# Optimization experiments

Hardware: AMD Instinct MI355X
Metric: run time of the kernel (lower is better)

Reference implementation:

```python
import jax, jax.numpy as jnp
import numpy as np

D_MODEL = 1024
N_STATE = 16
D_INNER = 2 * D_MODEL          # 2048
DT_RANK = (D_MODEL + 15) // 16  # 64 = ceil(d/16)
K_CONV = 4
B, L = 1, 1024


def setup_inputs() -> dict:
    key = jax.random.key(0)
    ks = jax.random.split(key, 9)
    s = lambda fan_in: 1.0 / np.sqrt(fan_in)
    x = jax.random.normal(ks[0], (B, L, D_MODEL), dtype=jnp.float32)
    W_in = jax.random.normal(ks[1], (D_MODEL, 2 * D_INNER), dtype=jnp.float32) * s(D_MODEL)
    conv_w = jax.random.normal(ks[2], (D_INNER, K_CONV), dtype=jnp.float32) * s(K_CONV)
    conv_b = jnp.zeros((D_INNER,), dtype=jnp.float32)
    W_x = jax.random.normal(ks[3], (D_INNER, DT_RANK + 2 * N_STATE), dtype=jnp.float32) * s(D_INNER)
    W_dt = jax.random.normal(ks[4], (DT_RANK, D_INNER), dtype=jnp.float32) * s(DT_RANK)
    b_dt = jax.random.normal(ks[5], (D_INNER,), dtype=jnp.float32) * 0.01
    # A_log initialized as log(1..N) repeated over d_inner, as in __init__
    A_log = jnp.log(jnp.broadcast_to(jnp.arange(1, N_STATE + 1, dtype=jnp.float32), (D_INNER, N_STATE)))
    D = jnp.ones((D_INNER,), dtype=jnp.float32)
    W_out = jax.random.normal(ks[6], (D_INNER, D_MODEL), dtype=jnp.float32) * s(D_INNER)
    return {"x": x, "W_in": W_in, "conv_w": conv_w, "conv_b": conv_b,
            "W_x": W_x, "W_dt": W_dt, "b_dt": b_dt, "A_log": A_log,
            "D": D, "W_out": W_out}


def _causal_dw_conv(x, w, b):
    # x: [B,L,C], w: [C,K], b: [C]; causal depthwise conv (pad left K-1)
    K = w.shape[1]
    xp = jnp.pad(x, ((0, 0), (K - 1, 0), (0, 0)))
    Lx = x.shape[1]
    out = b
    for k in range(K):  # small fixed K=4
        out = out + xp[:, k:k + Lx, :] * w[:, k]
    return out


def _selective_scan(u, delta, A, Bm, Cm, D):
    # u,delta: [B,L,Di]; A: [Di,N]; Bm,Cm: [B,L,N]; D: [Di]
    dA = jnp.exp(delta[..., None] * A)                      # [B,L,Di,N]
    dBu = delta[..., None] * Bm[:, :, None, :] * u[..., None]
    dA_t = jnp.moveaxis(dA, 1, 0)    # [L,B,Di,N]
    dBu_t = jnp.moveaxis(dBu, 1, 0)
    C_t = jnp.moveaxis(Cm, 1, 0)     # [L,B,N]

    def step(h, inp):
        dA_i, dBu_i, C_i = inp
        h = dA_i * h + dBu_i
        y = jnp.einsum('bdn,bn->bd', h, C_i)
        return h, y

    h0 = jnp.zeros(u.shape[:1] + A.shape, dtype=u.dtype)  # [B,Di,N]
    _, ys = jax.lax.scan(step, h0, (dA_t, dBu_t, C_t))
    y = jnp.moveaxis(ys, 0, 1)       # [B,L,Di]
    return y + u * D


def reference(x, W_in, conv_w, conv_b, W_x, W_dt, b_dt, A_log, D, W_out):
    silu = jax.nn.silu
    x_and_res = x @ W_in                                   # [B,L,2*Di]
    x_in, res = jnp.split(x_and_res, 2, axis=-1)
    x_conv = silu(_causal_dw_conv(x_in, conv_w, conv_b))   # [B,L,Di]
    x_dbl = x_conv @ W_x                                   # [B,L,dt_rank+2N]
    dt, Bm, Cm = jnp.split(x_dbl, [DT_RANK, DT_RANK + N_STATE], axis=-1)
    delta = jax.nn.softplus(dt @ W_dt + b_dt)              # [B,L,Di]
    A = -jnp.exp(A_log)                                    # [Di,N]
    y = _selective_scan(x_conv, delta, A, Bm, Cm, D)
    return (y * silu(res)) @ W_out                         # [B,L,d_model]
```

## Files before the change

kernel.cpp:

```cpp
#include <hip/hip_runtime.h>

typedef unsigned short u16;
typedef unsigned int u32;
typedef __attribute__((ext_vector_type(8))) short bf16x8;
typedef __attribute__((ext_vector_type(4))) float f32x4;

#define LSEQ 1024
#define NSL 8

__device__ __forceinline__ float b2f(u16 v) { return __uint_as_float(((u32)v) << 16); }
__device__ __forceinline__ u16 f2b(float f) {
    u32 x = __float_as_uint(f);
    return (u16)((x + 0x7fffu + ((x >> 16) & 1u)) >> 16);
}
__device__ __forceinline__ float rdf(const void* p, size_t i, int f) {
    return f ? b2f(((const u16*)p)[i]) : ((const float*)p)[i];
}
__device__ __forceinline__ float fsig(float x) {
    return __builtin_amdgcn_rcpf(1.f + __expf(-x));
}

typedef const __attribute__((address_space(1))) u32* gp_t;
typedef __attribute__((address_space(3))) u32* lp_t;
__device__ __forceinline__ void gload16(const u16* g, u16* lds_wave_base) {
    __builtin_amdgcn_global_load_lds((gp_t)g, (lp_t)lds_wave_base, 16, 0, 0);
}

__global__ __launch_bounds__(256) void prep_k(const void* __restrict__ x,
                                              const void* __restrict__ W_in,
                                              const void* __restrict__ W_out,
                                              const void* __restrict__ W_x,
                                              const void* __restrict__ W_dt,
                                              u16* __restrict__ xb,
                                              u16* __restrict__ W_in_t,
                                              u16* __restrict__ W_out_t,
                                              u16* __restrict__ W_x_t,
                                              u16* __restrict__ W_dt_t,
                                              int* __restrict__ scan_flags,
                                              int* __restrict__ flag) {
    __shared__ int cnt;
    __shared__ __align__(8) u16 tile[32][36];
    if (threadIdx.x == 0) cnt = 0;
    __syncthreads();
    const u16* xu = (const u16*)x;
    int c = 0;
#pragma unroll
    for (int j = 0; j < 8; ++j) {
        u16 u = xu[threadIdx.x * 8 + j];
        int e = (u >> 7) & 0xFF;
        c += (e == 0 || (e >= 100 && e <= 140)) ? 1 : 0;
    }
    atomicAdd(&cnt, c);
    __syncthreads();
    const int f = (cnt >= 1638) ? 1 : 0;
    if (blockIdx.x == 0 && threadIdx.x == 0) *flag = f;

    int blk = blockIdx.x;
    if (blk < 1024) {
        if (blk == 0) {
            scan_flags[threadIdx.x] = 0;
            scan_flags[256 + threadIdx.x] = 0;
        }
        int i = (blk * 256 + threadIdx.x) * 4;
        ushort4 o;
        if (f) {
            o = *(const ushort4*)(xu + i);
        } else {
            float4 v = *(const float4*)((const float*)x + i);
            o = make_ushort4(f2b(v.x), f2b(v.y), f2b(v.z), f2b(v.w));
        }
        *(ushort4*)(xb + i) = o;
        return;
    }
    blk -= 1024;
    const void* src; u16* dst; int R, Cn, nbc, t;
    if (blk < 4096)      { src = W_in;  dst = W_in_t;  R = 1024; Cn = 4096; nbc = 128; t = blk; }
    else if (blk < 6144) { src = W_out; dst = W_out_t; R = 2048; Cn = 1024; nbc = 32;  t = blk - 4096; }
    else if (blk < 6400) { src = W_x;   dst = W_x_t;   R = 2048; Cn = 96;   nbc = 4;   t = blk - 6144; }
    else                 { src = W_dt;  dst = W_dt_t;  R = 64;   Cn = 2048; nbc = 64;  t = blk - 6400; }
    int br = t / nbc, bc = t - br * nbc;
    int r0 = br * 32, c0 = bc * 32;
    {
        int ty = threadIdx.x >> 3, tx4 = (threadIdx.x & 7) << 2;
        u16 o0 = 0, o1 = 0, o2 = 0, o3 = 0;
        if (c0 + tx4 < Cn) {
            size_t off = (size_t)(r0 + ty) * Cn + c0 + tx4;
            if (f) {
                ushort4 u = *(const ushort4*)((const u16*)src + off);
                o0 = u.x; o1 = u.y; o2 = u.z; o3 = u.w;
            } else {
                float4 v = *(const float4*)((const float*)src + off);
                o0 = f2b(v.x); o1 = f2b(v.y); o2 = f2b(v.z); o3 = f2b(v.w);
            }
        }
        *(ushort4*)(&tile[ty][tx4]) = make_ushort4(o0, o1, o2, o3);
    }
    __syncthreads();
    {
        int cc = threadIdx.x >> 3, r4 = (threadIdx.x & 7) << 2;
        ushort4 o = make_ushort4(tile[r4][cc], tile[r4 + 1][cc], tile[r4 + 2][cc], tile[r4 + 3][cc]);
        *(ushort4*)(dst + (size_t)(c0 + cc) * R + r0 + r4) = o;
    }
}

template <int MT, int NT, int OUT_MODE>
__global__ __launch_bounds__(256) void gemm_bt(const u16* __restrict__ A,
                                               const u16* __restrict__ Bt,
                                               void* __restrict__ C,
                                               int M, int N, int K,
                                               const int* __restrict__ flag) {
    constexpr int BM = 32 * MT, BN = 32 * NT;
    __shared__ __align__(16) u16 As[2][2 * BM * 32];
    __shared__ __align__(16) u16 Bs[2][2 * BN * 32];
    const int tid = threadIdx.x;
    const int w = tid >> 6, lane = tid & 63;
    const int wm = w & 1, wn = w >> 1;
    const int m_blk = blockIdx.x * BM, n_blk = blockIdx.y * BN;
    const int lm = lane & 15, lq = lane >> 4;
    const int sr = lane >> 2, sc = (lane & 3) << 3;
    const int f = (OUT_MODE == 2) ? flag[0] : 0;

    f32x4 acc[MT][NT];
#pragma unroll
    for (int i = 0; i < MT; ++i)
#pragma unroll
        for (int j = 0; j < NT; ++j) acc[i][j] = (f32x4){0.f, 0.f, 0.f, 0.f};

    auto stage = [&](int buf, int kb) {
#pragma unroll
        for (int cch = 0; cch < 2; ++cch) {
#pragma unroll
            for (int i = 0; i < BM / 64; ++i) {
                int row = i * 64 + w * 16;
                gload16(A + (size_t)(m_blk + row + sr) * K + kb + cch * 32 + sc,
                        &As[buf][cch * BM * 32 + row * 32]);
            }
#pragma unroll
            for (int i = 0; i < BN / 64; ++i) {
                int row = i * 64 + w * 16;
                gload16(Bt + (size_t)(n_blk + row + sr) * K + kb + cch * 32 + sc,
                        &Bs[buf][cch * BN * 32 + row * 32]);
            }
        }
    };
    auto compute = [&](int buf) {
#pragma unroll
        for (int cch = 0; cch < 2; ++cch) {
            bf16x8 af[MT], bf[NT];
#pragma unroll
            for (int tm = 0; tm < MT; ++tm)
                af[tm] = *(const bf16x8*)(&As[buf][cch * BM * 32 +
                                                   (wm * 16 * MT + tm * 16 + lm) * 32 + lq * 8]);
#pragma unroll
            for (int tn = 0; tn < NT; ++tn)
                bf[tn] = *(const bf16x8*)(&Bs[buf][cch * BN * 32 +
                                                   (wn * 16 * NT + tn * 16 + lm) * 32 + lq * 8]);
#pragma unroll
            for (int tm = 0; tm < MT; ++tm)
#pragma unroll
                for (int tn = 0; tn < NT; ++tn)
                    acc[tm][tn] = __builtin_amdgcn_mfma_f32_16x16x32_bf16(af[tm], bf[tn],
                                                                          acc[tm][tn], 0, 0, 0);
        }
    };

    stage(0, 0);
    __syncthreads();
    int cur = 0;
    for (int kb = 64; kb < K; kb += 64) {
        stage(cur ^ 1, kb);
        compute(cur);
        __syncthreads();
        cur ^= 1;
    }
    compute(cur);

#pragma unroll
    for (int tm = 0; tm < MT; ++tm)
#pragma unroll
        for (int tn = 0; tn < NT; ++tn)
#pragma unroll
            for (int r = 0; r < 4; ++r) {
                int row = m_blk + wm * 16 * MT + tm * 16 + lq * 4 + r;
                int col = n_blk + wn * 16 * NT + tn * 16 + lm;
                float v = acc[tm][tn][r];
                if (OUT_MODE == 1) {
                    ((u16*)C)[(size_t)row * N + col] = f2b(v);
                } else {
                    if (f) ((u16*)C)[(size_t)row * N + col] = f2b(v);
                    else   ((float*)C)[(size_t)row * N + col] = v;
                }
            }
}

__global__ __launch_bounds__(256) void gemm2_conv_k(const u16* __restrict__ xz,
                                                    const u16* __restrict__ Bt,
                                                    float* __restrict__ parts,
                                                    u16* __restrict__ xconv,
                                                    const void* __restrict__ cw,
                                                    const void* __restrict__ cb,
                                                    const int* __restrict__ flag) {
    constexpr int MT = 2, NT = 4;
    constexpr int BM = 64, BN = 128, K = 2048, KLEN = 256;
    __shared__ __align__(16) u16 As[2][2 * BM * 32];
    __shared__ __align__(16) u16 Bs[2][2 * BN * 32];
    __shared__ __align__(16) float cws[KLEN * 4];
    __shared__ float cbs[KLEN];
    const int tid = threadIdx.x;
    const int w = tid >> 6, lane = tid & 63;
    const int wm = w & 1, wn = w >> 1;
    const int m_blk = blockIdx.x * BM;
    const int kb0 = blockIdx.z * KLEN;
    const int lm = lane & 15, lq = lane >> 4;
    const int sr = lane >> 2, sc = (lane & 3) << 3;
    const int f = flag[0];

    {
#pragma unroll
        for (int k = 0; k < 4; ++k) cws[tid * 4 + k] = rdf(cw, (size_t)(kb0 + tid) * 4 + k, f);
        cbs[tid] = rdf(cb, kb0 + tid, f);
    }
    __syncthreads();

    f32x4 acc[MT][NT];
#pragma unroll
    for (int i = 0; i < MT; ++i)
#pragma unroll
        for (int j = 0; j < NT; ++j) acc[i][j] = (f32x4){0.f, 0.f, 0.f, 0.f};

    const int arow = tid >> 2;
    const int acg = (tid & 3) << 3;
    const int trow = m_blk + arow;

    auto bstage = [&](int buf, int kb) {
#pragma unroll
        for (int cch = 0; cch < 2; ++cch)
#pragma unroll
            for (int i = 0; i < BN / 64; ++i) {
                int row = i * 64 + w * 16;
                gload16(Bt + (size_t)(row + sr) * K + kb + cch * 32 + sc,
                        &Bs[buf][cch * BN * 32 + row * 32]);
            }
    };
    auto astage = [&](int buf, int cch, int kbase) {
        const int d = kbase + acg;
        const int dl = kbase - kb0 + acg;
        bf16x8 xv[4];
#pragma unroll
        for (int kk = 0; kk < 4; ++kk) {
            bf16x8 zz = {0, 0, 0, 0, 0, 0, 0, 0};
            int tt = trow + kk - 3;
            xv[kk] = (tt >= 0) ? *(const bf16x8*)(xz + (size_t)tt * 4096 + d) : zz;
        }
        bf16x8 rv;
#pragma unroll
        for (int j = 0; j < 8; ++j) {
            f32x4 wv = *(const f32x4*)(cws + (dl + j) * 4);
            float a = cbs[dl + j];
#pragma unroll
            for (int kk = 0; kk < 4; ++kk) a += b2f((u16)xv[kk][j]) * wv[kk];
            rv[j] = (short)f2b(a * fsig(a));
        }
        *(bf16x8*)(&As[buf][cch * BM * 32 + arow * 32 + acg]) = rv;
        *(bf16x8*)(xconv + (size_t)trow * 2048 + d) = rv;
    };
    auto compute = [&](int buf) {
#pragma unroll
        for (int cch = 0; cch < 2; ++cch) {
            bf16x8 af[MT], bf[NT];
#pragma unroll
            for (int tm = 0; tm < MT; ++tm)
                af[tm] = *(const bf16x8*)(&As[buf][cch * BM * 32 +
                                                   (wm * 32 + tm * 16 + lm) * 32 + lq * 8]);
#pragma unroll
            for (int tn = 0; tn < NT; ++tn)
                bf[tn] = *(const bf16x8*)(&Bs[buf][cch * BN * 32 +
                                                   (wn * 64 + tn * 16 + lm) * 32 + lq * 8]);
#pragma unroll
            for (int tm = 0; tm < MT; ++tm)
#pragma unroll
                for (int tn = 0; tn < NT; ++tn)
                    acc[tm][tn] = __builtin_amdgcn_mfma_f32_16x16x32_bf16(af[tm], bf[tn],
                                                                          acc[tm][tn], 0, 0, 0);
        }
    };

    bstage(0, kb0);
    astage(0, 0, kb0);
    astage(0, 1, kb0 + 32);
    __syncthreads();
    int cur = 0;
    for (int kb = kb0 + 64; kb < kb0 + KLEN; kb += 64) {
        bstage(cur ^ 1, kb);
        astage(cur ^ 1, 0, kb);
        astage(cur ^ 1, 1, kb + 32);
        compute(cur);
        __syncthreads();
        cur ^= 1;
    }
    compute(cur);

#pragma unroll
    for (int tm = 0; tm < MT; ++tm)
#pragma unroll
        for (int tn = 0; tn < NT; ++tn)
#pragma unroll
            for (int r = 0; r < 4; ++r) {
                int row = m_blk + wm * 32 + tm * 16 + lq * 4 + r;
                int col = wn * 64 + tn * 16 + lm;
                parts[(size_t)blockIdx.z * 131072 + (size_t)row * 128 + col] = acc[tm][tn][r];
            }
}

__device__ __forceinline__ void delta_tile(const float* __restrict__ parts,
                                           const u16* __restrict__ Wdt,
                                           const void* __restrict__ bias,
                                           int f, int t0, int d0,
                                           u16* As2, u16* Bs2, float (*dlt)[128],
                                           int tid, int w, int lm, int lq, int sr, int sc) {
#pragma unroll
    for (int cch = 0; cch < 2; ++cch)
#pragma unroll
        for (int i = 0; i < 2; ++i) {
            int row = i * 64 + w * 16;
            gload16(Wdt + (size_t)(d0 + row + sr) * 64 + cch * 32 + sc,
                    Bs2 + cch * 4096 + row * 32);
        }
    {
        int arow = tid >> 3, acg = (tid & 7) << 3;
        f32x4 s0 = {0.f, 0.f, 0.f, 0.f}, s1 = {0.f, 0.f, 0.f, 0.f};
#pragma unroll
        for (int sl = 0; sl < NSL; ++sl) {
            const float* p = parts + (size_t)sl * 131072 + (size_t)(t0 + arow) * 128 + acg;
            s0 += *(const f32x4*)p;
            s1 += *(const f32x4*)(p + 4);
        }
        bf16x8 rv;
#pragma unroll
        for (int j = 0; j < 4; ++j) {
            rv[j] = (short)f2b(s0[j]);
            rv[4 + j] = (short)f2b(s1[j]);
        }
        *(bf16x8*)(As2 + (acg >> 5) * 1024 + arow * 32 + (acg & 31)) = rv;
    }
    __syncthreads();

    f32x4 dacc[2][2];
#pragma unroll
    for (int i = 0; i < 2; ++i)
#pragma unroll
        for (int j = 0; j < 2; ++j) dacc[i][j] = (f32x4){0.f, 0.f, 0.f, 0.f};
#pragma unroll
    for (int cch = 0; cch < 2; ++cch) {
        bf16x8 af[2], bf[2];
#pragma unroll
        for (int tm = 0; tm < 2; ++tm)
            af[tm] = *(const bf16x8*)(As2 + cch * 1024 + (tm * 16 + lm) * 32 + lq * 8);
#pragma unroll
        for (int tn = 0; tn < 2; ++tn)
            bf[tn] = *(const bf16x8*)(Bs2 + cch * 4096 + (w * 32 + tn * 16 + lm) * 32 + lq * 8);
#pragma unroll
        for (int tm = 0; tm < 2; ++tm)
#pragma unroll
            for (int tn = 0; tn < 2; ++tn)
                dacc[tm][tn] = __builtin_amdgcn_mfma_f32_16x16x32_bf16(af[tm], bf[tn],
                                                                       dacc[tm][tn], 0, 0, 0);
    }
#pragma unroll
    for (int tm = 0; tm < 2; ++tm)
#pragma unroll
        for (int tn = 0; tn < 2; ++tn)
#pragma unroll
            for (int r = 0; r < 4; ++r) {
                int row = tm * 16 + lq * 4 + r;
                int col = w * 32 + tn * 16 + lm;
                float b = rdf(bias, d0 + col, f);
                float t2 = dacc[tm][tn][r] + b;
                dlt[row][col] = fmaxf(t2, 0.f) + __logf(1.f + __expf(-fabsf(t2)));
            }
    __syncthreads();
}

__global__ __launch_bounds__(256) void scan_fused_k(const u16* __restrict__ xc,
                                                    const float* __restrict__ parts,
                                                    const u16* __restrict__ Wdt,
                                                    const void* __restrict__ bias,
                                                    const u16* __restrict__ xz,
                                                    const void* __restrict__ A_log,
                                                    const void* __restrict__ Dvp,
                                                    float* __restrict__ Acar,
                                                    float* __restrict__ Bcar,
                                                    int* __restrict__ flags,
                                                    u16* __restrict__ yg,
                                                    const int* __restrict__ flag) {
    __shared__ __align__(16) u16 As2[2 * 32 * 32];
    __shared__ __align__(16) u16 Bs2[2 * 128 * 32];
    __shared__ float dlt[32][128];
    __shared__ float BCs[32][32];
    const int f = *flag;
    const int tid = threadIdx.x, b = blockIdx.x;
    const int w = tid >> 6, lane = tid & 63;
    const int lm = lane & 15, lq = lane >> 4;
    const int sr = lane >> 2, sc = (lane & 3) << 3;
    const int c = b >> 4, dblk = b & 15;
    const int d0 = dblk * 128;
    const int t0 = c * 32;
    {
        int idx = tid * 4;
        int tl = idx >> 5, col = idx & 31;
        f32x4 s = {0.f, 0.f, 0.f, 0.f};
#pragma unroll
        for (int sl = 0; sl < NSL; ++sl)
            s += *(const f32x4*)(parts + (size_t)sl * 131072 + (size_t)(t0 + tl) * 128 + 64 + col);
        *(f32x4*)&BCs[tl][col] = s;
    }
    delta_tile(parts, Wdt, bias, f, t0, d0, As2, Bs2, dlt, tid, w, lm, lq, sr, sc);

    const int dl = tid >> 1, nh = tid & 1;
    const int d = d0 + dl, n0 = nh << 3;

    float A[8], P[8], h[8];
#pragma unroll
    for (int j = 0; j < 8; ++j) {
        A[j] = -__expf(rdf(A_log, d * 16 + n0 + j, f));
        P[j] = 1.f;
        h[j] = 0.f;
    }
#pragma unroll 4
    for (int i = 0; i < 32; ++i) {
        int t = t0 + i;
        float de = dlt[i][dl];
        float dBu = de * b2f(xc[t * 2048 + d]);
        f32x4 Bv0 = *(const f32x4*)&BCs[i][n0];
        f32x4 Bv1 = *(const f32x4*)&BCs[i][n0 + 4];
#pragma unroll
        for (int j = 0; j < 8; ++j) {
            float Bv = (j < 4) ? Bv0[j & 3] : Bv1[j & 3];
            float a = __expf(de * A[j]);
            h[j] = a * h[j] + Bv * dBu;
            P[j] *= a;
        }
    }
    size_t base = (size_t)c * 32768 + d * 16 + n0;
    {
        f32x4 pa0 = {P[0], P[1], P[2], P[3]}, pa1 = {P[4], P[5], P[6], P[7]};
        f32x4 hb0 = {h[0], h[1], h[2], h[3]}, hb1 = {h[4], h[5], h[6], h[7]};
        *(f32x4*)(Acar + base) = pa0;
        *(f32x4*)(Acar + base + 4) = pa1;
        *(f32x4*)(Bcar + base) = hb0;
        *(f32x4*)(Bcar + base + 4) = hb1;
    }
    __syncthreads();
    if (tid == 0)
        __hip_atomic_store(&flags[b], 1, __ATOMIC_RELEASE, __HIP_MEMORY_SCOPE_AGENT);

    float H[8];
#pragma unroll
    for (int j = 0; j < 8; ++j) H[j] = 0.f;
    if (c > 0) {
        if (tid < c) {
            while (__hip_atomic_load(&flags[tid * 16 + dblk], __ATOMIC_ACQUIRE,
                                     __HIP_MEMORY_SCOPE_AGENT) == 0)
                __builtin_amdgcn_s_sleep(1);
        }
        __syncthreads();
        for (int cc = 0; cc < c; ++cc) {
            size_t cb = (size_t)cc * 32768 + d * 16 + n0;
            f32x4 a0 = *(const f32x4*)(Acar + cb);
            f32x4 a1 = *(const f32x4*)(Acar + cb + 4);
            f32x4 b0 = *(const f32x4*)(Bcar + cb);
            f32x4 b1 = *(const f32x4*)(Bcar + cb + 4);
#pragma unroll
            for (int j = 0; j < 4; ++j) {
                H[j] = a0[j] * H[j] + b0[j];
                H[4 + j] = a1[j] * H[4 + j] + b1[j];
            }
        }
    }

#pragma unroll
    for (int j = 0; j < 8; ++j) h[j] = H[j];
    float Dd = rdf(Dvp, d, f);
#pragma unroll 4
    for (int i = 0; i < 32; ++i) {
        int t = t0 + i;
        float de = dlt[i][dl];
        float u = b2f(xc[t * 2048 + d]);
        float dBu = de * u;
        f32x4 Bv0 = *(const f32x4*)&BCs[i][n0];
        f32x4 Bv1 = *(const f32x4*)&BCs[i][n0 + 4];
        f32x4 Cv0 = *(const f32x4*)&BCs[i][16 + n0];
        f32x4 Cv1 = *(const f32x4*)&BCs[i][20 + n0];
        float p = 0.f;
#pragma unroll
        for (int j = 0; j < 8; ++j) {
            float Bv = (j < 4) ? Bv0[j & 3] : Bv1[j & 3];
            float Cv = (j < 4) ? Cv0[j & 3] : Cv1[j & 3];
            float a = __expf(de * A[j]);
            h[j] = a * h[j] + Bv * dBu;
            p += h[j] * Cv;
        }
        p += __shfl_xor(p, 1);
        if (nh == 0) {
            float r = b2f(xz[(size_t)t * 4096 + 2048 + d]);
            float yt = p + u * Dd;
            yg[t * 2048 + d] = f2b(yt * r * fsig(r));
        }
    }
}

__global__ __launch_bounds__(256) void gemm3_red_k(const float* __restrict__ parts,
                                                   const u16* __restrict__ Bt,
                                                   float* __restrict__ delta,
                                                   const void* __restrict__ bias,
                                                   const int* __restrict__ flag) {
    constexpr int MT = 2, NT = 2, BM = 64, BN = 64, K = 64;
    __shared__ __align__(16) u16 As[2 * BM * 32];
    __shared__ __align__(16) u16 Bs[2 * BN * 32];
    const int tid = threadIdx.x;
    const int w = tid >> 6, lane = tid & 63;
    const int wm = w & 1, wn = w >> 1;
    const int m_blk = blockIdx.x * BM, n_blk = blockIdx.y * BN;
    const int lm = lane & 15, lq = lane >> 4;
    const int sr = lane >> 2, sc = (lane & 3) << 3;
    const int f = flag[0];

    f32x4 acc[MT][NT];
#pragma unroll
    for (int i = 0; i < MT; ++i)
#pragma unroll
        for (int j = 0; j < NT; ++j) acc[i][j] = (f32x4){0.f, 0.f, 0.f, 0.f};

    const int arow = tid >> 2;
    const int acg = (tid & 3) << 3;

#pragma unroll
    for (int cch = 0; cch < 2; ++cch) {
        int row = w * 16;
        gload16(Bt + (size_t)(n_blk + row + sr) * K + cch * 32 + sc, &Bs[cch * BN * 32 + row * 32]);
    }
#pragma unroll
    for (int cch = 0; cch < 2; ++cch) {
        f32x4 s0 = {0.f, 0.f, 0.f, 0.f}, s1 = {0.f, 0.f, 0.f, 0.f};
#pragma unroll
        for (int sl = 0; sl < NSL; ++sl) {
            const float* p = parts + (size_t)sl * 131072 + (size_t)(m_blk + arow) * 128 + cch * 32 + acg;
            s0 += *(const f32x4*)p;
            s1 += *(const f32x4*)(p + 4);
        }
        bf16x8 rv;
#pragma unroll
        for (int j = 0; j < 4; ++j) {
            rv[j] = (short)f2b(s0[j]);
            rv[4 + j] = (short)f2b(s1[j]);
        }
        *(bf16x8*)(&As[cch * BM * 32 + arow * 32 + acg]) = rv;
    }
    __syncthreads();

#pragma unroll
    for (int cch = 0; cch < 2; ++cch) {
        bf16x8 af[MT], bf[NT];
#pragma unroll
        for (int tm = 0; tm < MT; ++tm)
            af[tm] = *(const bf16x8*)(&As[cch * BM * 32 + (wm * 32 + tm * 16 + lm) * 32 + lq * 8]);
#pragma unroll
        for (int tn = 0; tn < NT; ++tn)
            bf[tn] = *(const bf16x8*)(&Bs[cch * BN * 32 + (wn * 32 + tn * 16 + lm) * 32 + lq * 8]);
#pragma unroll
        for (int tm = 0; tm < MT; ++tm)
#pragma unroll
            for (int tn = 0; tn < NT; ++tn)
                acc[tm][tn] = __builtin_amdgcn_mfma_f32_16x16x32_bf16(af[tm], bf[tn],
                                                                      acc[tm][tn], 0, 0, 0);
    }

#pragma unroll
    for (int tm = 0; tm < MT; ++tm)
#pragma unroll
        for (int tn = 0; tn < NT; ++tn)
#pragma unroll
            for (int r = 0; r < 4; ++r) {
                int row = m_blk + wm * 32 + tm * 16 + lq * 4 + r;
                int col = n_blk + wn * 32 + tn * 16 + lm;
                float b = rdf(bias, col, f);
                float t2 = acc[tm][tn][r] + b;
                float sp = fmaxf(t2, 0.f) + __logf(1.f + __expf(-fabsf(t2)));
                delta[(size_t)row * 2048 + col] = sp;
            }
}

__global__ __launch_bounds__(256) void scan_k(const float* __restrict__ delta,
                                              const u16* __restrict__ xc,
                                              const float* __restrict__ parts,
                                              const u16* __restrict__ xz,
                                              const void* __restrict__ A_log,
                                              const void* __restrict__ Dvp,
                                              u16* __restrict__ yg,
                                              const int* __restrict__ flag) {
    int f = *flag;
    int g = blockIdx.x * 256 + threadIdx.x;
    int d = g >> 4, n = g & 15;
    float A = -__expf(rdf(A_log, d * 16 + n, f));
    float Dd = rdf(Dvp, d, f);
    float h = 0.f;
    for (int t = 0; t < LSEQ; ++t) {
        float de = delta[t * 2048 + d];
        float u = b2f(xc[t * 2048 + d]);
        float Bv = 0.f, Cv = 0.f;
#pragma unroll
        for (int sl = 0; sl < NSL; ++sl) {
            Bv += parts[(size_t)sl * 131072 + (size_t)t * 128 + 64 + n];
            Cv += parts[(size_t)sl * 131072 + (size_t)t * 128 + 80 + n];
        }
        h = __expf(de * A) * h + (de * Bv) * u;
        float p = h * Cv;
        p += __shfl_xor(p, 1);
        p += __shfl_xor(p, 2);
        p += __shfl_xor(p, 4);
        p += __shfl_xor(p, 8);
        if (n == 0) {
            float r = b2f(xz[(size_t)t * 4096 + 2048 + d]);
            float yt = p + u * Dd;
            yg[t * 2048 + d] = f2b(yt * r * fsig(r));
        }
    }
}

extern "C" void kernel_launch(void* const* d_in, const int* in_sizes, int n_in,
                              void* d_out, int out_size, void* d_ws, size_t ws_size,
                              hipStream_t stream) {
    const void* x      = d_in[0];
    const void* W_in   = d_in[1];
    const void* conv_w = d_in[2];
    const void* conv_b = d_in[3];
    const void* W_x    = d_in[4];
    const void* W_dt   = d_in[5];
    const void* b_dt   = d_in[6];
    const void* A_log  = d_in[7];
    const void* Dv     = d_in[8];
    const void* W_out  = d_in[9];

    char* ws = (char*)d_ws;
    u16*   xz     = (u16*)(ws);
    u16*   xconv  = (u16*)(ws + 8388608);
    float* parts  = (float*)(ws + 12582912);
    u16*   W_in_t = (u16*)(ws + 16777216);
    u16*   yg     = (u16*)(ws + 25165824);
    u16*   xb     = (u16*)(ws + 25165824);
    u16*   W_x_t  = (u16*)(ws + 29360128);
    u16*   W_dt_t = (u16*)(ws + 29884416);
    u16*   W_out_t= (u16*)(ws + 30146560);
    int*   flag   = (int*)(ws + 34340864);
    float* Acar   = (float*)(ws + 34340992);
    float* Bcar   = (float*)(ws + 38535296);
    int*   sflags = (int*)(ws + 42729600);
    float* dfb    = (float*)(ws + 34340992);
    const bool chunked_ok = (ws_size >= 42731648);

    prep_k<<<7552, 256, 0, stream>>>(x, W_in, W_out, W_x, W_dt,
                                     xb, W_in_t, W_out_t, W_x_t, W_dt_t, sflags, flag);
    gemm_bt<2, 4, 1><<<dim3(16, 32), 256, 0, stream>>>(xb, W_in_t, (void*)xz,
                                                       1024, 4096, 1024, flag);
    gemm2_conv_k<<<dim3(16, 1, 8), 256, 0, stream>>>(xz, W_x_t, parts, xconv,
                                                     conv_w, conv_b, flag);

    if (chunked_ok) {
        scan_fused_k<<<512, 256, 0, stream>>>(xconv, parts, W_dt_t, b_dt, xz, A_log, Dv,
                                              Acar, Bcar, sflags, yg, flag);
    } else {
        gemm3_red_k<<<dim3(16, 32), 256, 0, stream>>>(parts, W_dt_t, dfb, b_dt, flag);
        scan_k<<<128, 256, 0, stream>>>(dfb, xconv, parts, xz, A_log, Dv, yg, flag);
    }

    gemm_bt<2, 2, 2><<<dim3(16, 16), 256, 0, stream>>>(yg, W_out_t, d_out,
                                                       1024, 1024, 2048, flag);
}
```

Baseline: 224.2 us.

## Split fused chunked scan into two kernels instead of inter-block flag spinning

Replaces the single fused scan kernel, which published per-chunk carries and spin-waited on global flags for earlier chunks, with two launches. The first computes delta, the B/C projections and the chunk-local carries, and spills delta and B/C to global memory. The second reloads them, combines the prefix carries and produces outputs. This removes the inter-block busy-wait serialization and any reliance on co-residency, at the cost of an extra launch and an extra round trip of the delta tensor through global memory.

```diff
diff --git a/kernel.cpp b/kernel.cpp
--- a/kernel.cpp
+++ b/kernel.cpp
@@ -36,7 +36,6 @@
                                               u16* __restrict__ W_out_t,
                                               u16* __restrict__ W_x_t,
                                               u16* __restrict__ W_dt_t,
-                                              int* __restrict__ scan_flags,
                                               int* __restrict__ flag) {
     __shared__ int cnt;
     __shared__ __align__(8) u16 tile[32][36];
@@ -57,10 +56,6 @@
 
     int blk = blockIdx.x;
     if (blk < 1024) {
-        if (blk == 0) {
-            scan_flags[threadIdx.x] = 0;
-            scan_flags[256 + threadIdx.x] = 0;
-        }
         int i = (blk * 256 + threadIdx.x) * 4;
         ushort4 o;
         if (f) {
@@ -381,22 +376,20 @@
     __syncthreads();
 }
 
-__global__ __launch_bounds__(256) void scan_fused_k(const u16* __restrict__ xc,
-                                                    const float* __restrict__ parts,
-                                                    const u16* __restrict__ Wdt,
-                                                    const void* __restrict__ bias,
-                                                    const u16* __restrict__ xz,
-                                                    const void* __restrict__ A_log,
-                                                    const void* __restrict__ Dvp,
-                                                    float* __restrict__ Acar,
-                                                    float* __restrict__ Bcar,
-                                                    int* __restrict__ flags,
-                                                    u16* __restrict__ yg,
-                                                    const int* __restrict__ flag) {
+__global__ __launch_bounds__(256) void scan1_k(const u16* __restrict__ xc,
+                                               const float* __restrict__ parts,
+                                               const u16* __restrict__ Wdt,
+                                               const void* __restrict__ bias,
+                                               const void* __restrict__ A_log,
+                                               float* __restrict__ Acar,
+                                               float* __restrict__ Bcar,
+                                               float* __restrict__ deltag,
+                                               float* __restrict__ bcg,
+                                               const int* __restrict__ flag) {
     __shared__ __align__(16) u16 As2[2 * 32 * 32];
     __shared__ __align__(16) u16 Bs2[2 * 128 * 32];
-    __shared__ float dlt[32][128];
-    __shared__ float BCs[32][32];
+    __shared__ __align__(16) float dlt[32][128];
+    __shared__ __align__(16) float BCs[32][32];
     const int f = *flag;
     const int tid = threadIdx.x, b = blockIdx.x;
     const int w = tid >> 6, lane = tid & 63;
@@ -416,9 +409,20 @@
     }
     delta_tile(parts, Wdt, bias, f, t0, d0, As2, Bs2, dlt, tid, w, lm, lq, sr, sc);
 
+#pragma unroll
+    for (int k = 0; k < 4; ++k) {
+        int kk = tid + k * 256;
+        int row = kk >> 5, col4 = (kk & 31) << 2;
+        *(f32x4*)(deltag + (size_t)(t0 + row) * 2048 + d0 + col4) = *(const f32x4*)&dlt[row][col4];
+    }
+    if (dblk == 0) {
+        int idx = tid * 4;
+        int tl = idx >> 5, col = idx & 31;
+        *(f32x4*)(bcg + c * 1024 + tl * 32 + col) = *(const f32x4*)&BCs[tl][col];
+    }
+
     const int dl = tid >> 1, nh = tid & 1;
     const int d = d0 + dl, n0 = nh << 3;
-
     float A[8], P[8], h[8];
 #pragma unroll
     for (int j = 0; j < 8; ++j) {
@@ -441,45 +445,66 @@
             P[j] *= a;
         }
     }
+    f32x4 pa0 = {P[0], P[1], P[2], P[3]}, pa1 = {P[4], P[5], P[6], P[7]};
+    f32x4 hb0 = {h[0], h[1], h[2], h[3]}, hb1 = {h[4], h[5], h[6], h[7]};
     size_t base = (size_t)c * 32768 + d * 16 + n0;
+    *(f32x4*)(Acar + base) = pa0;
+    *(f32x4*)(Acar + base + 4) = pa1;
+    *(f32x4*)(Bcar + base) = hb0;
+    *(f32x4*)(Bcar + base + 4) = hb1;
+}
+
+__global__ __launch_bounds__(256) void scan3_k(const u16* __restrict__ xc,
+                                               const float* __restrict__ deltag,
+                                               const float* __restrict__ bcg,
+                                               const u16* __restrict__ xz,
+                                               const void* __restrict__ A_log,
+                                               const void* __restrict__ Dvp,
+                                               const float* __restrict__ Acar,
+                                               const float* __restrict__ Bcar,
+                                               u16* __restrict__ yg,
+                                               const int* __restrict__ flag) {
+    __shared__ __align__(16) float dlt[32][128];
+    __shared__ __align__(16) float BCs[32][32];
+    const int f = *flag;
+    const int tid = threadIdx.x, b = blockIdx.x;
+    const int c = b >> 4;
+    const int d0 = (b & 15) * 128;
+    const int t0 = c * 32;
     {
-        f32x4 pa0 = {P[0], P[1], P[2], P[3]}, pa1 = {P[4], P[5], P[6], P[7]};
-        f32x4 hb0 = {h[0], h[1], h[2], h[3]}, hb1 = {h[4], h[5], h[6], h[7]};
-        *(f32x4*)(Acar + base) = pa0;
-        *(f32x4*)(Acar + base + 4) = pa1;
-        *(f32x4*)(Bcar + base) = hb0;
-        *(f32x4*)(Bcar + base + 4) = hb1;
-    }
-    __syncthreads();
-    if (tid == 0)
-        __hip_atomic_store(&flags[b], 1, __ATOMIC_RELEASE, __HIP_MEMORY_SCOPE_AGENT);
-
-    float H[8];
-#pragma unroll
-    for (int j = 0; j < 8; ++j) H[j] = 0.f;
-    if (c > 0) {
-        if (tid < c) {
-            while (__hip_atomic_load(&flags[tid * 16 + dblk], __ATOMIC_ACQUIRE,
-                                     __HIP_MEMORY_SCOPE_AGENT) == 0)
-                __builtin_amdgcn_s_sleep(1);
-        }
-        __syncthreads();
-        for (int cc = 0; cc < c; ++cc) {
-            size_t cb = (size_t)cc * 32768 + d * 16 + n0;
-            f32x4 a0 = *(const f32x4*)(Acar + cb);
-            f32x4 a1 = *(const f32x4*)(Acar + cb + 4);
-            f32x4 b0 = *(const f32x4*)(Bcar + cb);
-            f32x4 b1 = *(const f32x4*)(Bcar + cb + 4);
-#pragma unroll
-            for (int j = 0; j < 4; ++j) {
-                H[j] = a0[j] * H[j] + b0[j];
-                H[4 + j] = a1[j] * H[4 + j] + b1[j];
-            }
-        }
-    }
-
-#pragma unroll
-    for (int j = 0; j < 8; ++j) h[j] = H[j];
+        int idx = tid * 4;
+        int tl = idx >> 5, col = idx & 31;
+        *(f32x4*)&BCs[tl][col] = *(const f32x4*)(bcg + c * 1024 + tl * 32 + col);
+    }
+#pragma unroll
+    for (int k = 0; k < 4; ++k) {
+        int kk = tid + k * 256;
+        int row = kk >> 5, col4 = (kk & 31) << 2;
+        *(f32x4*)&dlt[row][col4] = *(const f32x4*)(deltag + (size_t)(t0 + row) * 2048 + d0 + col4);
+    }
+    __syncthreads();
+
+    const int dl = tid >> 1, nh = tid & 1;
+    const int d = d0 + dl, n0 = nh << 3;
+    float A[8], h[8];
+#pragma unroll
+    for (int j = 0; j < 8; ++j) {
+        A[j] = -__expf(rdf(A_log, d * 16 + n0 + j, f));
+        h[j] = 0.f;
+    }
+    for (int cc = 0; cc < c; ++cc) {
+        size_t cb = (size_t)cc * 32768 + d * 16 + n0;
+        f32x4 a0 = *(const f32x4*)(Acar + cb);
+        f32x4 a1 = *(const f32x4*)(Acar + cb + 4);
+        f32x4 b0 = *(const f32x4*)(Bcar + cb);
+        f32x4 b1 = *(const f32x4*)(Bcar + cb + 4);
+#pragma unroll
+        for (int j = 0; j < 4; ++j) {
+            h[j] = a0[j] * h[j] + b0[j];
+            h[4 + j] = a1[j] * h[4 + j] + b1[j];
+        }
+    }
+
     float Dd = rdf(Dvp, d, f);
 #pragma unroll 4
     for (int i = 0; i < 32; ++i) {
@@ -654,20 +679,23 @@
     int*   flag   = (int*)(ws + 34340864);
     float* Acar   = (float*)(ws + 34340992);
     float* Bcar   = (float*)(ws + 38535296);
-    int*   sflags = (int*)(ws + 42729600);
+    float* deltag = (float*)(ws + 42729600);
+    float* bcg    = (float*)(ws + 51118208);
     float* dfb    = (float*)(ws + 34340992);
-    const bool chunked_ok = (ws_size >= 42731648);
+    const bool chunked_ok = (ws_size >= 51249280);
 
     prep_k<<<7552, 256, 0, stream>>>(x, W_in, W_out, W_x, W_dt,
-                                     xb, W_in_t, W_out_t, W_x_t, W_dt_t, sflags, flag);
+                                     xb, W_in_t, W_out_t, W_x_t, W_dt_t, flag);
     gemm_bt<2, 4, 1><<<dim3(16, 32), 256, 0, stream>>>(xb, W_in_t, (void*)xz,
                                                        1024, 4096, 1024, flag);
     gemm2_conv_k<<<dim3(16, 1, 8), 256, 0, stream>>>(xz, W_x_t, parts, xconv,
                                                      conv_w, conv_b, flag);
 
     if (chunked_ok) {
-        scan_fused_k<<<512, 256, 0, stream>>>(xconv, parts, W_dt_t, b_dt, xz, A_log, Dv,
-                                              Acar, Bcar, sflags, yg, flag);
+        scan1_k<<<512, 256, 0, stream>>>(xconv, parts, W_dt_t, b_dt, A_log, Acar, Bcar,
+                                         deltag, bcg, flag);
+        scan3_k<<<512, 256, 0, stream>>>(xconv, deltag, bcg, xz, A_log, Dv,
+                                         Acar, Bcar, yg, flag);
     } else {
         gemm3_red_k<<<dim3(16, 32), 256, 0, stream>>>(parts, W_dt_t, dfb, b_dt, flag);
         scan_k<<<128, 256, 0, stream>>>(dfb, xconv, parts, xz, A_log, Dv, yg, flag);
```

Result: faster. 205.3 us (-8.4%).
